# Performance work log

Measured on AMD Instinct MI355X. Metric: run time of the kernel, lower is better.

## Reference

```python
import jax, jax.numpy as jnp
import numpy as np

SIGMA = 0.3
EPS = 1e-8  # torch CosineSimilarity eps


def _log_prob(v):
    # Normal(loc=1, scale=SIGMA).log_prob(v)
    log_z = jnp.log(SIGMA) + 0.5 * jnp.log(2.0 * jnp.pi)
    return -((v - 1.0) ** 2) / (2.0 * SIGMA ** 2) - log_z


def setup_inputs() -> dict:
    key = jax.random.key(0)
    k1, k2 = jax.random.split(key)
    ex = jax.random.normal(k1, (16384, 256), dtype=jnp.float32)
    ey = jax.random.normal(k2, (16384, 256), dtype=jnp.float32)
    return {"ex": ex, "ey": ey}


def reference(ex, ey):
    # cosine similarity matrix C[n, m] between all rows of ex and ey
    xn = ex / jnp.maximum(jnp.linalg.norm(ex, axis=-1, keepdims=True), EPS)
    yn = ey / jnp.maximum(jnp.linalg.norm(ey, axis=-1, keepdims=True), EPS)
    C = xn @ yn.T  # [N, M]
    # dim=None branch: entropy over row-max and col-max similarities
    C1 = _log_prob(jnp.max(C, axis=-1))  # [N]
    C2 = _log_prob(jnp.max(C, axis=0))   # [M]
    e1 = -jnp.sum(jnp.exp(C1) * C1)
    e2 = -jnp.sum(jnp.exp(C2) * C2)
    return (e1, e2)
```

## Files before the change

### kernel.cpp

```cpp
#include <hip/hip_runtime.h>


typedef _Float16 f16x8 __attribute__((ext_vector_type(8)));
typedef _Float16 f16x4 __attribute__((ext_vector_type(4)));
typedef float f32x16 __attribute__((ext_vector_type(16)));

#define NROWS 16384
#define KDIM 256

__device__ inline unsigned f2mono(float f) {
  unsigned b = __float_as_uint(f);
  return (b & 0x80000000u) ? ~b : (b | 0x80000000u);
}
__device__ inline float mono2f(unsigned u) {
  return __uint_as_float((u & 0x80000000u) ? (u ^ 0x80000000u) : ~u);
}

template <int CTRL>
__device__ inline float dppmax(float v) {
  int r = __builtin_amdgcn_update_dpp(0, __float_as_int(v), CTRL, 0xf, 0xf, true);
  return fmaxf(v, __int_as_float(r));
}

__global__ __launch_bounds__(256) void normalize_k(
    const float* __restrict__ ex, const float* __restrict__ ey,
    _Float16* __restrict__ xn, _Float16* __restrict__ yn) {
  const int lane = threadIdx.x & 63;
  const int row = blockIdx.x * 4 + (threadIdx.x >> 6);
  const float* src;
  _Float16* dst;
  int r;
  if (row < NROWS) {
    src = ex + (size_t)row * KDIM;
    dst = xn;
    r = row;
  } else {
    src = ey + (size_t)(row - NROWS) * KDIM;
    dst = yn;
    r = row - NROWS;
  }
  float4 v = *reinterpret_cast<const float4*>(src + lane * 4);
  float ss = v.x * v.x + v.y * v.y + v.z * v.z + v.w * v.w;
#pragma unroll
  for (int m = 1; m <= 32; m <<= 1) ss += __shfl_xor(ss, m, 64);
  float inv = 1.0f / fmaxf(sqrtf(ss), 1e-8f);
  f16x4 o;
  o[0] = (_Float16)(v.x * inv);
  o[1] = (_Float16)(v.y * inv);
  o[2] = (_Float16)(v.z * inv);
  o[3] = (_Float16)(v.w * inv);
  const int kb = lane >> 2, h = (lane >> 1) & 1, sub = lane & 1;
  const size_t chunk = (size_t)(r >> 5) * 16 + kb;
  const size_t off = chunk * 512 + (h * 32 + (r & 31)) * 8 + sub * 4;
  *reinterpret_cast<f16x4*>(dst + off) = o;
}

__global__ __launch_bounds__(512, 2) void gemm_max_k(
    const _Float16* __restrict__ Xf, const _Float16* __restrict__ Yf,
    unsigned* __restrict__ rmax, unsigned* __restrict__ cmax) {
  __shared__ unsigned red[512];

  const int tid = threadIdx.x;
  const int lane = tid & 63;
  const int wid = tid >> 6;
  const int wr = wid >> 2;
  const int wc = wid & 3;

  const int bid = blockIdx.x;
  const int wg = (bid & 7) * 512 + (bid >> 3);
  const int tm = wg >> 6;
  const int tn = wg & 63;

  red[tid] = 0;
  __syncthreads();

  const _Float16* abase =
      Xf + (size_t)(tm * 8 + wr * 4) * 8192 + lane * 8;
  const _Float16* bbase =
      Yf + (size_t)(tn * 8 + wc * 2) * 8192 + lane * 8;

  f32x16 acc[4][2] = {};

#pragma unroll
  for (int kt = 0; kt < 16; ++kt) {
    f16x8 a0 = *(const f16x8*)(abase + 0 * 8192 + kt * 512);
    f16x8 a1 = *(const f16x8*)(abase + 1 * 8192 + kt * 512);
    f16x8 a2 = *(const f16x8*)(abase + 2 * 8192 + kt * 512);
    f16x8 a3 = *(const f16x8*)(abase + 3 * 8192 + kt * 512);
    f16x8 b0 = *(const f16x8*)(bbase + 0 * 8192 + kt * 512);
    f16x8 b1 = *(const f16x8*)(bbase + 1 * 8192 + kt * 512);
    acc[0][0] = __builtin_amdgcn_mfma_f32_32x32x16_f16(a0, b0, acc[0][0], 0, 0, 0);
    acc[0][1] = __builtin_amdgcn_mfma_f32_32x32x16_f16(a0, b1, acc[0][1], 0, 0, 0);
    acc[1][0] = __builtin_amdgcn_mfma_f32_32x32x16_f16(a1, b0, acc[1][0], 0, 0, 0);
    acc[1][1] = __builtin_amdgcn_mfma_f32_32x32x16_f16(a1, b1, acc[1][1], 0, 0, 0);
    acc[2][0] = __builtin_amdgcn_mfma_f32_32x32x16_f16(a2, b0, acc[2][0], 0, 0, 0);
    acc[2][1] = __builtin_amdgcn_mfma_f32_32x32x16_f16(a2, b1, acc[2][1], 0, 0, 0);
    acc[3][0] = __builtin_amdgcn_mfma_f32_32x32x16_f16(a3, b0, acc[3][0], 0, 0, 0);
    acc[3][1] = __builtin_amdgcn_mfma_f32_32x32x16_f16(a3, b1, acc[3][1], 0, 0, 0);
  }

#pragma unroll
  for (int m = 0; m < 4; ++m) {
#pragma unroll
    for (int r = 0; r < 16; ++r) {
      float v = fmaxf(acc[m][0][r], acc[m][1][r]);
      v = dppmax<0x128>(v);
      v = dppmax<0x124>(v);
      v = dppmax<0x122>(v);
      v = dppmax<0x121>(v);
      v = fmaxf(v, __shfl_xor(v, 16, 64));
      if ((lane & 31) == 0)
        atomicMax(&red[wr * 128 + m * 32 + (r & 3) + 8 * (r >> 2) +
                       4 * (lane >> 5)],
                  f2mono(v));
    }
  }
#pragma unroll
  for (int n = 0; n < 2; ++n) {
    float v = acc[0][n][0];
#pragma unroll
    for (int m = 0; m < 4; ++m)
#pragma unroll
      for (int r = 0; r < 16; ++r) v = fmaxf(v, acc[m][n][r]);
    v = fmaxf(v, __shfl_xor(v, 32, 64));
    if (lane < 32) atomicMax(&red[256 + wc * 64 + n * 32 + lane], f2mono(v));
  }
  __syncthreads();

  if (tid < 256)
    atomicMax(&rmax[tm * 256 + tid], red[tid]);
  else
    atomicMax(&cmax[tn * 256 + (tid - 256)], red[tid]);
}

__global__ __launch_bounds__(256) void finalize_k(
    const unsigned* __restrict__ rmax, const unsigned* __restrict__ cmax,
    float* __restrict__ out) {
  const unsigned* src = (blockIdx.x == 0) ? rmax : cmax;
  float sum = 0.0f;
  for (int i = threadIdx.x; i < NROWS; i += 256) {
    float v = mono2f(src[i]);
    float d = v - 1.0f;
    float lp = fmaf(-d * d, 5.5555555556f, 0.2850342717f);
    sum += expf(lp) * lp;
  }
#pragma unroll
  for (int m = 1; m <= 32; m <<= 1) sum += __shfl_xor(sum, m, 64);
  __shared__ float partial[4];
  if ((threadIdx.x & 63) == 0) partial[threadIdx.x >> 6] = sum;
  __syncthreads();
  if (threadIdx.x == 0)
    out[blockIdx.x] = -(partial[0] + partial[1] + partial[2] + partial[3]);
}

extern "C" void kernel_launch(void* const* d_in, const int* in_sizes, int n_in,
                              void* d_out, int out_size, void* d_ws, size_t ws_size,
                              hipStream_t stream) {
  const float* ex = (const float*)d_in[0];
  const float* ey = (const float*)d_in[1];
  char* wsb = (char*)d_ws;
  _Float16* xn = (_Float16*)wsb;
  _Float16* yn = (_Float16*)(wsb + 8388608);
  unsigned* rmax = (unsigned*)(wsb + 16777216);
  unsigned* cmax = (unsigned*)(wsb + 16777216 + 65536);

  (void)hipMemsetAsync(wsb + 16777216, 0, 131072, stream);
  normalize_k<<<8192, 256, 0, stream>>>(ex, ey, xn, yn);
  gemm_max_k<<<4096, 512, 0, stream>>>(xn, yn, rmax, cmax);
  finalize_k<<<2, 256, 0, stream>>>(rmax, cmax, (float*)d_out);
}
```

Measured before the change: 396.5 us.

## Stage operands through LDS with triple-buffered async global-to-LDS loads

Replaces direct per-wave global loads of the A/B fragments with cooperative global_load_lds copies into a three-stage LDS ring buffer, prefetching two k-steps ahead and using vmcnt waits plus barriers. Each wave now loads one row-chunk instead of redundantly fetching four A and two B chunks, which cuts duplicated global/L2 traffic and overlaps memory with MFMA. It also remaps block indices to 8x8 tile groups for L2 locality and raises wave priority around the MFMA block. The cost is about 50KB of LDS per block, which may limit occupancy to two blocks, plus a barrier on every k-step.

```diff
diff --git a/kernel.cpp b/kernel.cpp
--- a/kernel.cpp
+++ b/kernel.cpp
@@ -7,6 +7,12 @@
 
 #define NROWS 16384
 #define KDIM 256
+
+__device__ inline void gl_lds16(const void* g, void* l) {
+  __builtin_amdgcn_global_load_lds(
+      (const __attribute__((address_space(1))) void*)g,
+      (__attribute__((address_space(3))) void*)l, 16, 0, 0);
+}
 
 __device__ inline unsigned f2mono(float f) {
   unsigned b = __float_as_uint(f);
@@ -58,7 +64,7 @@
 __global__ __launch_bounds__(512, 2) void gemm_max_k(
     const _Float16* __restrict__ Xf, const _Float16* __restrict__ Yf,
     unsigned* __restrict__ rmax, unsigned* __restrict__ cmax) {
-  __shared__ unsigned red[512];
+  __shared__ __align__(16) char smem[51200];
 
   const int tid = threadIdx.x;
   const int lane = tid & 63;
@@ -67,28 +73,55 @@
   const int wc = wid & 3;
 
   const int bid = blockIdx.x;
-  const int wg = (bid & 7) * 512 + (bid >> 3);
-  const int tm = wg >> 6;
-  const int tn = wg & 63;
-
+  const int x = bid & 7;
+  const int lid = bid >> 3;
+  const int sq = lid >> 6;
+  const int r8 = lid & 63;
+  const int tm = x * 8 + (r8 >> 3);
+  const int tn = sq * 8 + (r8 & 7);
+
+  const _Float16* xa = Xf + (size_t)(tm * 8 + wid) * 8192 + lane * 8;
+  const _Float16* ya = Yf + (size_t)(tn * 8 + wid) * 8192 + lane * 8;
+
+  unsigned* red = (unsigned*)(smem + 49152);
   red[tid] = 0;
   __syncthreads();
 
-  const _Float16* abase =
-      Xf + (size_t)(tm * 8 + wr * 4) * 8192 + lane * 8;
-  const _Float16* bbase =
-      Yf + (size_t)(tn * 8 + wc * 2) * 8192 + lane * 8;
+  auto stage = [&](int u) {
+    const int bo = (u % 3) * 16384;
+    gl_lds16(xa + u * 512, smem + bo + wid * 1024 + lane * 16);
+    gl_lds16(ya + u * 512, smem + bo + 8192 + wid * 1024 + lane * 16);
+  };
+
+  int aoff[4], boff[2];
+#pragma unroll
+  for (int m = 0; m < 4; ++m) aoff[m] = (wr * 4 + m) * 1024 + lane * 16;
+#pragma unroll
+  for (int n = 0; n < 2; ++n) boff[n] = 8192 + (wc * 2 + n) * 1024 + lane * 16;
 
   f32x16 acc[4][2] = {};
 
+  stage(0);
+  stage(1);
+
 #pragma unroll
   for (int kt = 0; kt < 16; ++kt) {
-    f16x8 a0 = *(const f16x8*)(abase + 0 * 8192 + kt * 512);
-    f16x8 a1 = *(const f16x8*)(abase + 1 * 8192 + kt * 512);
-    f16x8 a2 = *(const f16x8*)(abase + 2 * 8192 + kt * 512);
-    f16x8 a3 = *(const f16x8*)(abase + 3 * 8192 + kt * 512);
-    f16x8 b0 = *(const f16x8*)(bbase + 0 * 8192 + kt * 512);
-    f16x8 b1 = *(const f16x8*)(bbase + 1 * 8192 + kt * 512);
+    if (kt < 15)
+      asm volatile("s_waitcnt vmcnt(2)" ::: "memory");
+    else
+      asm volatile("s_waitcnt vmcnt(0)" ::: "memory");
+    __builtin_amdgcn_sched_barrier(0);
+    __builtin_amdgcn_s_barrier();
+    __builtin_amdgcn_sched_barrier(0);
+    if (kt + 2 < 16) stage(kt + 2);
+    const int bo = (kt % 3) * 16384;
+    f16x8 a0 = *(const f16x8*)(smem + bo + aoff[0]);
+    f16x8 a1 = *(const f16x8*)(smem + bo + aoff[1]);
+    f16x8 a2 = *(const f16x8*)(smem + bo + aoff[2]);
+    f16x8 a3 = *(const f16x8*)(smem + bo + aoff[3]);
+    f16x8 b0 = *(const f16x8*)(smem + bo + boff[0]);
+    f16x8 b1 = *(const f16x8*)(smem + bo + boff[1]);
+    __builtin_amdgcn_s_setprio(1);
     acc[0][0] = __builtin_amdgcn_mfma_f32_32x32x16_f16(a0, b0, acc[0][0], 0, 0, 0);
     acc[0][1] = __builtin_amdgcn_mfma_f32_32x32x16_f16(a0, b1, acc[0][1], 0, 0, 0);
     acc[1][0] = __builtin_amdgcn_mfma_f32_32x32x16_f16(a1, b0, acc[1][0], 0, 0, 0);
@@ -97,6 +130,7 @@
     acc[2][1] = __builtin_amdgcn_mfma_f32_32x32x16_f16(a2, b1, acc[2][1], 0, 0, 0);
     acc[3][0] = __builtin_amdgcn_mfma_f32_32x32x16_f16(a3, b0, acc[3][0], 0, 0, 0);
     acc[3][1] = __builtin_amdgcn_mfma_f32_32x32x16_f16(a3, b1, acc[3][1], 0, 0, 0);
+    __builtin_amdgcn_s_setprio(0);
   }
 
 #pragma unroll
```

Result: faster. 342.6 us (-13.6%).
